# Optimization experiments

Hardware: AMD Instinct MI355X
Metric: run time of the kernel (lower is better)

Reference implementation:

```python
import jax, jax.numpy as jnp
import numpy as np

NUM_EXPERTS = 8
TOP_K = 2
LORA_ALPHA = 2.0
LORA_RANK = 16
D_MODEL = 2048
D_HIDDEN = 5632


def setup_inputs() -> dict:
    key = jax.random.key(0)
    ks = jax.random.split(key, 11)
    B, S, D, H, E, R = 2, 1024, D_MODEL, D_HIDDEN, NUM_EXPERTS, LORA_RANK
    sd = 1.0 / np.sqrt(D)
    sh = 1.0 / np.sqrt(H)
    x = jax.random.normal(ks[0], (B, S, D), jnp.float32)
    gate_w = jax.random.normal(ks[1], (E, D), jnp.float32) * sd   # router Linear(D->E), no bias
    w_up = jax.random.normal(ks[2], (H, D), jnp.float32) * sd     # up_proj.weight
    w_gate = jax.random.normal(ks[3], (H, D), jnp.float32) * sd   # gate_proj.weight
    w_down = jax.random.normal(ks[4], (D, H), jnp.float32) * sh   # down_proj.weight
    up_A = jax.random.normal(ks[5], (E, R, D), jnp.float32) * sd
    up_B = jax.random.normal(ks[6], (E, H, R), jnp.float32) * 0.02
    gate_A = jax.random.normal(ks[7], (E, R, D), jnp.float32) * sd
    gate_B = jax.random.normal(ks[8], (E, H, R), jnp.float32) * 0.02
    down_A = jax.random.normal(ks[9], (E, R, H), jnp.float32) * sh
    down_B = jax.random.normal(ks[10], (E, D, R), jnp.float32) * 0.02
    return {"x": x, "gate_w": gate_w, "w_up": w_up, "w_gate": w_gate,
            "w_down": w_down, "up_A": up_A, "up_B": up_B,
            "gate_A": gate_A, "gate_B": gate_B, "down_A": down_A, "down_B": down_B}


def reference(x, gate_w, w_up, w_gate, w_down, up_A, up_B, gate_A, gate_B, down_A, down_B):
    B, S, D = x.shape
    H = w_up.shape[0]
    # router: logits [B,S,E], top-k over experts (last dim)
    gate_logits = jnp.einsum('bsd,ed->bse', x, gate_w)
    topw, sel = jax.lax.top_k(gate_logits, TOP_K)            # [B,S,k]
    # NOTE: source applies softmax over dim=1 (the SEQUENCE axis) -- reproduced faithfully
    topw = jax.nn.softmax(topw.astype(jnp.float32), axis=1).astype(x.dtype)
    xt = x.reshape(-1, D)                                    # [T, D]
    wf = topw.reshape(-1, TOP_K)                             # [T, k]
    sf = sel.reshape(-1, TOP_K)                              # [T, k]
    # shared base projections computed once for all tokens
    base_up = xt @ w_up.T                                    # [T, H]
    base_gate = xt @ w_gate.T                                # [T, H]
    mixed_h = jnp.zeros((xt.shape[0], H), x.dtype)
    lora_down = jnp.zeros_like(xt)
    # loop over fixed small expert count; low-rank LoRA deltas applied without
    # materializing full merged weights (same math by linearity of matmul)
    for e in range(NUM_EXPERTS):
        c = jnp.sum(jnp.where(sf == e, wf, 0.0), axis=1)     # [T] routing weight (0 if not routed)
        lo_up = LORA_ALPHA * ((xt @ up_A[e].T) @ up_B[e].T)
        lo_gate = LORA_ALPHA * ((xt @ gate_A[e].T) @ gate_B[e].T)
        h_e = jax.nn.silu(base_up + lo_up) * (base_gate + lo_gate)  # [T, H]
        ch = c[:, None] * h_e
        mixed_h = mixed_h + ch
        lora_down = lora_down + LORA_ALPHA * ((ch @ down_A[e].T) @ down_B[e].T)
    out = mixed_h @ w_down.T + lora_down                     # base down GEMM done once on mixed hidden
    return out.reshape(B, S, D)
```

## Files before the change

### kernel.cpp

```cpp
#include <hip/hip_runtime.h>
#include <hip/hip_fp16.h>
#include <cmath>

#define TOKENS 2048
#define DMODEL 2048
#define DHID   5632
#define NEXP   8
#define RANK   16
#define LALPHA 2.0f

typedef __attribute__((ext_vector_type(4))) float f32x4;
typedef __attribute__((ext_vector_type(8))) short s16x8;
typedef __attribute__((ext_vector_type(4))) short s16x4;
typedef __attribute__((ext_vector_type(8))) _Float16 f16x8;

__device__ __forceinline__ short f2bf(float f){
  unsigned u = __float_as_uint(f);
  u += 0x7fffu + ((u >> 16) & 1u);
  return (short)(u >> 16);
}
__device__ __forceinline__ short f2h(float f){
  return (short)__half_as_ushort(__float2half(f));
}

struct Stage { const short* s0; const short* s1; short* d0; short* d1; };

__device__ __forceinline__ Stage mk_stage(const short* g, long ld, short* t, int tid){
  Stage st;
  const int L0 = tid,      r0 = L0>>2, c0 = ((L0&3) - (r0>>1)) & 3;
  const int L1 = 256+tid,  r1 = L1>>2, c1 = ((L1&3) - (r1>>1)) & 3;
  st.s0 = g + (long)r0*ld + c0*8;  st.d0 = t + L0*8;
  st.s1 = g + (long)r1*ld + c1*8;  st.d1 = t + L1*8;
  return st;
}
__device__ __forceinline__ void do_stage(const Stage& st, int k0){
  __builtin_amdgcn_global_load_lds((const __attribute__((address_space(1))) void*)(st.s0 + k0),
                                   (__attribute__((address_space(3))) void*)st.d0, 16, 0, 0);
  __builtin_amdgcn_global_load_lds((const __attribute__((address_space(1))) void*)(st.s1 + k0),
                                   (__attribute__((address_space(3))) void*)st.d1, 16, 0, 0);
}
__device__ __forceinline__ s16x8 fragb(const short* t, int row, int quad){
  const int p = (quad + (row>>1)) & 3;
  return *(const s16x8*)(t + (row*4 + p)*8);
}

struct Stage64 { const short* g; short* t; int off[4]; int dof; };

__device__ __forceinline__ Stage64 mk_stage64(const short* g, long ld, short* t, int tid){
  Stage64 st; st.g = g; st.t = t;
  #pragma unroll
  for(int p=0;p<4;p++){
    const int L = p*256 + tid;
    const int r = L>>3, cp = L&7;
    const int c = (cp - (r&7)) & 7;
    st.off[p] = r*(int)ld + c*8;
  }
  st.dof = tid*8;
  return st;
}
__device__ __forceinline__ void do_stage64(const Stage64& st, int k0){
  #pragma unroll
  for(int p=0;p<4;p++)
    __builtin_amdgcn_global_load_lds(
      (const __attribute__((address_space(1))) void*)(st.g + st.off[p] + k0),
      (__attribute__((address_space(3))) void*)(st.t + st.dof + p*2048), 16, 0, 0);
}
__device__ __forceinline__ s16x8 fragb64(const short* t, int row, int ksub, int quad){
  const int c = ksub*4 + quad;
  const int p = (c + (row&7)) & 7;
  return *(const s16x8*)(t + (row*8 + p)*8);
}
__device__ __forceinline__ f16x8 fragh64(const short* t, int row, int ksub, int quad){
  const int c = ksub*4 + quad;
  const int p = (c + (row&7)) & 7;
  return *(const f16x8*)(t + (row*8 + p)*8);
}

__global__ void k_cast(const float* __restrict__ x, const float* __restrict__ w_up,
                       const float* __restrict__ w_gate, const float* __restrict__ w_down,
                       const float* __restrict__ upA, const float* __restrict__ gateA,
                       const float* __restrict__ downA, const float* __restrict__ upB,
                       const float* __restrict__ gateB, const float* __restrict__ downB,
                       short* __restrict__ xb, short* __restrict__ wub, short* __restrict__ wgb,
                       short* __restrict__ wdb, short* __restrict__ daA, short* __restrict__ acat,
                       short* __restrict__ upBcat, short* __restrict__ gateBcat, short* __restrict__ wdbcat){
  const long e0 = 4194304, e1 = 15728640, e2 = 27262976, e3 = 38797312;
  const long e4 = 39518208, e5 = 40042496, e6 = 40763392, e7 = 41484288, e8 = 41746432;
  const long i = ((long)blockIdx.x*256 + threadIdx.x) * 4;
  if(i >= e8) return;
  const float* src; short* dst; long l; int fp16 = 0;
  if(i < e0){ src = x; dst = xb; l = i; }
  else if(i < e1){ src = w_up; dst = wub; l = i - e0; }
  else if(i < e2){ src = w_gate; dst = wgb; l = i - e1; }
  else if(i < e3){ src = w_down; dst = wdb; l = i - e2; }
  else if(i < e4){ src = downA; dst = daA; l = i - e3; }
  else if(i < e5){
    l = i - e4;
    const long c = l>>11;
    const long e = c>>5, pj = (c>>4)&1, r = c&15;
    src = (pj ? gateA : upA) + ((e*RANK + r)<<11) + (l&2047) - l;
    dst = acat;
  }
  else if(i < e6){
    l = i - e5;
    const long h = l>>7, c = l&127, e = c>>4, r = c&15;
    src = upB + ((e*DHID + h)*RANK + r) - l;
    dst = upBcat; fp16 = 1;
  }
  else if(i < e7){
    l = i - e6;
    const long h = l>>7, c = l&127, e = c>>4, r = c&15;
    src = gateB + ((e*DHID + h)*RANK + r) - l;
    dst = gateBcat; fp16 = 1;
  }
  else {
    l = i - e7;
    const long d = l>>7, c = l&127, e = c>>4, r = c&15;
    src = downB + ((e*DMODEL + d)*RANK + r) - l;
    dst = wdbcat; fp16 = 1;
  }
  const float4 v = *(const float4*)(src + l);
  s16x4 o;
  if(fp16){ o[0]=f2h(v.x); o[1]=f2h(v.y); o[2]=f2h(v.z); o[3]=f2h(v.w); }
  else    { o[0]=f2bf(v.x); o[1]=f2bf(v.y); o[2]=f2bf(v.z); o[3]=f2bf(v.w); }
  *(s16x4*)(dst + l) = o;
}

__global__ void k_router(const float* __restrict__ x, const float* __restrict__ gw,
                         int* __restrict__ sel, float* __restrict__ topv){
  const int t = blockIdx.x*4 + (threadIdx.x>>6);
  const int lane = threadIdx.x & 63;
  const float* xr = x + (long)t * DMODEL;
  float acc[NEXP];
  #pragma unroll
  for(int e=0;e<NEXP;e++) acc[e]=0.f;
  #pragma unroll
  for(int it=0; it<8; it++){
    const int d = it*256 + lane*4;
    const float4 xv = *(const float4*)(xr + d);
    #pragma unroll
    for(int e=0;e<NEXP;e++){
      const float4 wv = *(const float4*)(gw + e*DMODEL + d);
      acc[e] += xv.x*wv.x + xv.y*wv.y + xv.z*wv.z + xv.w*wv.w;
    }
  }
  #pragma unroll
  for(int e=0;e<NEXP;e++){
    #pragma unroll
    for(int off=32; off; off>>=1) acc[e] += __shfl_down(acc[e], off, 64);
  }
  if(lane==0){
    int i0=0;
    #pragma unroll
    for(int e=1;e<NEXP;e++) if(acc[e]>acc[i0]) i0=e;
    int i1=-1;
    #pragma unroll
    for(int e=0;e<NEXP;e++){ if(e==i0) continue; if(i1<0 || acc[e]>acc[i1]) i1=e; }
    sel[t*2+0]=i0; sel[t*2+1]=i1;
    topv[t*2+0]=acc[i0]; topv[t*2+1]=acc[i1];
  }
}

__global__ void k_softmax(const float* __restrict__ topv, float* __restrict__ cw){
  const int b = blockIdx.x >> 1, k = blockIdx.x & 1;
  const int base = b*1024;
  __shared__ float red[256];
  float v[4];
  float mx = -1e30f;
  #pragma unroll
  for(int i=0;i<4;i++){
    int s = threadIdx.x + i*256;
    v[i] = topv[(base+s)*2 + k];
    mx = fmaxf(mx, v[i]);
  }
  red[threadIdx.x]=mx; __syncthreads();
  for(int o=128;o;o>>=1){ if(threadIdx.x<o) red[threadIdx.x]=fmaxf(red[threadIdx.x],red[threadIdx.x+o]); __syncthreads(); }
  mx = red[0]; __syncthreads();
  float sum=0.f;
  #pragma unroll
  for(int i=0;i<4;i++){ v[i]=__expf(v[i]-mx); sum+=v[i]; }
  red[threadIdx.x]=sum; __syncthreads();
  for(int o=128;o;o>>=1){ if(threadIdx.x<o) red[threadIdx.x]+=red[threadIdx.x+o]; __syncthreads(); }
  const float inv = 1.f/red[0];
  #pragma unroll
  for(int i=0;i<4;i++){
    int s = threadIdx.x + i*256;
    cw[(base+s)*2+k] = v[i]*inv;
  }
}

__global__ __launch_bounds__(256,2) void k_rank(
    const short* __restrict__ xb, const short* __restrict__ acat, float* __restrict__ Rall){
  __shared__ __align__(16) short At[8192];
  __shared__ __align__(16) short Bt[8192];
  const int c0 = blockIdx.x*128, t0 = blockIdx.y*128;
  const int kbeg = blockIdx.z*256;
  const int tid = threadIdx.x, lane = tid&63, wave = tid>>6;
  const int wm=(wave>>1)*64, wn=(wave&1)*64, fr=lane&15, quad=lane>>4;
  f32x4 acc[4][4];
  #pragma unroll
  for(int i=0;i<4;i++)
    #pragma unroll
    for(int j=0;j<4;j++) acc[i][j]=(f32x4){0.f,0.f,0.f,0.f};
  const Stage64 sA = mk_stage64(xb + (long)t0*DMODEL, DMODEL, At, tid);
  const Stage64 sB = mk_stage64(acat + (long)c0*DMODEL, DMODEL, Bt, tid);
  for(int k0=kbeg; k0<kbeg+256; k0+=64){
    do_stage64(sA, k0); do_stage64(sB, k0);
    __syncthreads();
    #pragma unroll
    for(int s=0;s<2;s++){
      s16x8 af[4];
      #pragma unroll
      for(int i=0;i<4;i++) af[i] = fragb64(At, wm + i*16 + fr, s, quad);
      #pragma unroll
      for(int j=0;j<4;j++){
        const s16x8 bf = fragb64(Bt, wn + j*16 + fr, s, quad);
        #pragma unroll
        for(int i=0;i<4;i++)
          acc[i][j] = __builtin_amdgcn_mfma_f32_16x16x32_bf16(af[i], bf, acc[i][j], 0,0,0);
      }
    }
    __syncthreads();
  }
  #pragma unroll
  for(int i=0;i<4;i++)
    #pragma unroll
    for(int j=0;j<4;j++){
      const int rbase = wm + i*16 + quad*4, col = wn + j*16 + fr;
      #pragma unroll
      for(int reg=0;reg<4;reg++)
        atomicAdd(&Rall[(long)(t0+rbase+reg)*256 + c0 + col], acc[i][j][reg]);
    }
}

__global__ void k_rsel(const float* __restrict__ Rall, const int* __restrict__ sel,
                       short* __restrict__ RselU, short* __restrict__ RselG){
  const int idx = blockIdx.x*256 + threadIdx.x;
  const int c = idx & 127, t = (idx>>7) & (TOKENS-1), k = idx>>18;
  const int e = c>>4, r = c&15;
  const int s = sel[t*2+k];
  const int m = (e==s);
  RselU[idx] = f2h(m ? LALPHA*Rall[(long)t*256 + e*32 + r]      : 0.f);
  RselG[idx] = f2h(m ? LALPHA*Rall[(long)t*256 + e*32 + 16 + r] : 0.f);
}

__global__ __launch_bounds__(256,2) void k_lora(
    const short* __restrict__ RselU, const short* __restrict__ RselG,
    const short* __restrict__ upBcat, const short* __restrict__ gateBcat,
    short* __restrict__ LF){
  __shared__ __align__(16) short At[8192];
  __shared__ __align__(16) short Gt[8192];
  __shared__ __align__(16) short Bt[8192];
  const int h0 = blockIdx.x*128, t0 = blockIdx.y*128;
  const short* Rsel = blockIdx.z ? RselG : RselU;
  const short* Bcat = blockIdx.z ? gateBcat : upBcat;
  const int tid = threadIdx.x, lane = tid&63, wave = tid>>6;
  const int wm=(wave>>1)*64, wn=(wave&1)*64, fr=lane&15, quad=lane>>4;
  f32x4 l0[4][4], l1[4][4];
  #pragma unroll
  for(int i=0;i<4;i++)
    #pragma unroll
    for(int j=0;j<4;j++){ l0[i][j]=(f32x4){0.f,0.f,0.f,0.f}; l1[i][j]=l0[i][j]; }
  const Stage64 sB  = mk_stage64(Bcat + (long)h0*128, 128, Bt, tid);
  const Stage64 sR0 = mk_stage64(Rsel + (long)t0*128, 128, At, tid);
  const Stage64 sR1 = mk_stage64(Rsel + ((long)TOKENS + t0)*128, 128, Gt, tid);
  for(int k0=0; k0<128; k0+=64){
    do_stage64(sB, k0); do_stage64(sR0, k0); do_stage64(sR1, k0);
    __syncthreads();
    #pragma unroll
    for(int s=0;s<2;s++){
      f16x8 a0[4], a1[4];
      #pragma unroll
      for(int i=0;i<4;i++){ a0[i] = fragh64(At, wm + i*16 + fr, s, quad);
                            a1[i] = fragh64(Gt, wm + i*16 + fr, s, quad); }
      #pragma unroll
      for(int j=0;j<4;j++){
        const f16x8 bf = fragh64(Bt, wn + j*16 + fr, s, quad);
        #pragma unroll
        for(int i=0;i<4;i++){
          l0[i][j] = __builtin_amdgcn_mfma_f32_16x16x32_f16(a0[i], bf, l0[i][j], 0,0,0);
          l1[i][j] = __builtin_amdgcn_mfma_f32_16x16x32_f16(a1[i], bf, l1[i][j], 0,0,0);
        }
      }
    }
    __syncthreads();
  }
  short* o = LF + (((long)(blockIdx.y*44 + blockIdx.x)*256 + tid)*256) + blockIdx.z*128;
  #pragma unroll
  for(int i=0;i<4;i++){
    s16x8 p0a, p0b, p1a, p1b;
    #pragma unroll
    for(int r=0;r<4;r++){
      p0a[r]   = f2h(l0[i][0][r]); p0a[4+r] = f2h(l0[i][1][r]);
      p0b[r]   = f2h(l0[i][2][r]); p0b[4+r] = f2h(l0[i][3][r]);
      p1a[r]   = f2h(l1[i][0][r]); p1a[4+r] = f2h(l1[i][1][r]);
      p1b[r]   = f2h(l1[i][2][r]); p1b[4+r] = f2h(l1[i][3][r]);
    }
    *(s16x8*)(o + i*16)          = p0a;
    *(s16x8*)(o + i*16 + 8)      = p0b;
    *(s16x8*)(o + 64 + i*16)     = p1a;
    *(s16x8*)(o + 64 + i*16 + 8) = p1b;
  }
}

__global__ __launch_bounds__(256,2) void k_main(
    const short* __restrict__ xb, const short* __restrict__ wub, const short* __restrict__ wgb,
    const short* __restrict__ LF,
    const float* __restrict__ cw, unsigned short* __restrict__ ch, unsigned short* __restrict__ chsum){
  __shared__ __align__(16) short At[8192];
  __shared__ __align__(16) short Ut[8192];
  __shared__ __align__(16) short Gt[8192];
  __shared__ float cwv[128][2];
  const int h0 = blockIdx.x*128, t0 = blockIdx.y*128;
  const int tid = threadIdx.x, lane = tid&63, wave = tid>>6;
  const int wm=(wave>>1)*64, wn=(wave&1)*64, fr=lane&15, quad=lane>>4;
  { const int tl = tid>>1, k = tid&1; cwv[tl][k] = cw[(t0+tl)*2 + k]; }
  f32x4 au[4][4], ag[4][4];
  #pragma unroll
  for(int i=0;i<4;i++)
    #pragma unroll
    for(int j=0;j<4;j++){ au[i][j]=(f32x4){0.f,0.f,0.f,0.f}; ag[i][j]=au[i][j]; }
  const Stage64 sA = mk_stage64(xb + (long)t0*DMODEL, DMODEL, At, tid);
  const Stage64 sU = mk_stage64(wub + (long)h0*DMODEL, DMODEL, Ut, tid);
  const Stage64 sG = mk_stage64(wgb + (long)h0*DMODEL, DMODEL, Gt, tid);
  for(int k0=0; k0<DMODEL; k0+=64){
    do_stage64(sA, k0); do_stage64(sU, k0); do_stage64(sG, k0);
    __syncthreads();
    #pragma unroll
    for(int s=0;s<2;s++){
      s16x8 af[4];
      #pragma unroll
      for(int i=0;i<4;i++) af[i] = fragb64(At, wm + i*16 + fr, s, quad);
      #pragma unroll
      for(int j=0;j<4;j++){
        const s16x8 bu = fragb64(Ut, wn + j*16 + fr, s, quad);
        const s16x8 bg = fragb64(Gt, wn + j*16 + fr, s, quad);
        #pragma unroll
        for(int i=0;i<4;i++){
          au[i][j] = __builtin_amdgcn_mfma_f32_16x16x32_bf16(af[i], bu, au[i][j], 0,0,0);
          ag[i][j] = __builtin_amdgcn_mfma_f32_16x16x32_bf16(af[i], bg, ag[i][j], 0,0,0);
        }
      }
    }
    __syncthreads();
  }
  const short* Lf = LF + (((long)(blockIdx.y*44 + blockIdx.x)*256 + tid)*256);
  #pragma unroll
  for(int i=0;i<4;i++){
    f16x8 Uv0[2], Uv1[2], Gv0[2], Gv1[2];
    Uv0[0] = *(const f16x8*)(Lf + i*16);        Uv0[1] = *(const f16x8*)(Lf + i*16 + 8);
    Uv1[0] = *(const f16x8*)(Lf + 64 + i*16);   Uv1[1] = *(const f16x8*)(Lf + 64 + i*16 + 8);
    Gv0[0] = *(const f16x8*)(Lf + 128 + i*16);  Gv0[1] = *(const f16x8*)(Lf + 128 + i*16 + 8);
    Gv1[0] = *(const f16x8*)(Lf + 192 + i*16);  Gv1[1] = *(const f16x8*)(Lf + 192 + i*16 + 8);
    #pragma unroll
    for(int reg=0;reg<4;reg++){
      const int tl = wm + i*16 + quad*4 + reg;
      const float c0 = cwv[tl][0], c1 = cwv[tl][1];
      const long row0 = (long)(t0+tl)*DHID + h0;
      const long row1 = ((long)TOKENS + t0+tl)*DHID + h0;
      unsigned short* r0 = ch + row0;
      unsigned short* r1 = ch + row1;
      unsigned short* rs = chsum + row0;
      #pragma unroll
      for(int j=0;j<4;j++){
        const int hl = wn + j*16 + fr;
        const int q = (j&1)*4 + reg, hv = j>>1;
        const float u0 = au[i][j][reg] + (float)Uv0[hv][q];
        const float g0 = ag[i][j][reg] + (float)Gv0[hv][q];
        const float h0v = (u0 / (1.f + __expf(-u0))) * g0;
        const float u1 = au[i][j][reg] + (float)Uv1[hv][q];
        const float g1 = ag[i][j][reg] + (float)Gv1[hv][q];
        const float h1v = (u1 / (1.f + __expf(-u1))) * g1;
        const float v0 = c0*h0v, v1 = c1*h1v;
        r0[hl] = (unsigned short)f2bf(v0);
        r1[hl] = (unsigned short)f2bf(v1);
        rs[hl] = (unsigned short)f2bf(v0+v1);
      }
    }
  }
}

__global__ __launch_bounds__(256,4) void k_rd(
    const unsigned short* __restrict__ ch, const short* __restrict__ daA,
    float* __restrict__ RD){
  __shared__ __align__(16) short At[4096];
  __shared__ __align__(16) short Bt[4096];
  const int slot = blockIdx.x>>4, ks = blockIdx.x&15;
  const int t0 = blockIdx.y*128;
  const int tid = threadIdx.x, lane = tid&63, wave = tid>>6;
  const int wm=(wave>>1)*64, wn=(wave&1)*64, fr=lane&15, quad=lane>>4;
  f32x4 acc[4][4];
  #pragma unroll
  for(int i=0;i<4;i++)
    #pragma unroll
    for(int j=0;j<4;j++) acc[i][j]=(f32x4){0.f,0.f,0.f,0.f};
  const Stage sA = mk_stage((const short*)ch + ((long)slot*TOKENS + t0)*DHID, DHID, At, tid);
  const Stage sB = mk_stage(daA, DHID, Bt, tid);
  const int kbeg = ks*352;
  for(int kk=0; kk<352; kk+=32){
    do_stage(sA, kbeg+kk); do_stage(sB, kbeg+kk);
    __syncthreads();
    s16x8 af[4];
    #pragma unroll
    for(int i=0;i<4;i++) af[i] = fragb(At, wm + i*16 + fr, quad);
    #pragma unroll
    for(int j=0;j<4;j++){
      const s16x8 bf = fragb(Bt, wn + j*16 + fr, quad);
      #pragma unroll
      for(int i=0;i<4;i++)
        acc[i][j] = __builtin_amdgcn_mfma_f32_16x16x32_bf16(af[i], bf, acc[i][j], 0,0,0);
    }
    __syncthreads();
  }
  #pragma unroll
  for(int i=0;i<4;i++)
    #pragma unroll
    for(int j=0;j<4;j++){
      const int rbase = wm + i*16 + quad*4, col = wn + j*16 + fr;
      #pragma unroll
      for(int reg=0;reg<4;reg++)
        atomicAdd(&RD[((long)(t0+rbase+reg)*2 + slot)*128 + col], acc[i][j][reg]);
    }
}

__global__ void k_scatter(const float* __restrict__ RD, const int* __restrict__ sel,
                          __half* __restrict__ RDhat){
  const int idx = blockIdx.x*256 + threadIdx.x;
  const int t = idx>>7, c = idx&127, e = c>>4;
  const int s0 = sel[t*2], s1 = sel[t*2+1];
  float v = 0.f;
  if(e == s0) v = LALPHA * RD[((long)t*2+0)*128 + c];
  else if(e == s1) v = LALPHA * RD[((long)t*2+1)*128 + c];
  RDhat[idx] = __float2half(v);
}

__global__ __launch_bounds__(256,2) void k_down(
    const unsigned short* __restrict__ chsum, const short* __restrict__ wdb,
    const short* __restrict__ RDhat, const short* __restrict__ wdbcat,
    float* __restrict__ out){
  __shared__ __align__(16) short At[8192];
  __shared__ __align__(16) short Bt[8192];
  const int d0 = blockIdx.x*128, t0 = blockIdx.y*128, ks = blockIdx.z;
  const int tid = threadIdx.x, lane = tid&63, wave = tid>>6;
  const int wm=(wave>>1)*64, wn=(wave&1)*64, fr=lane&15, quad=lane>>4;
  f32x4 acc[4][4];
  #pragma unroll
  for(int i=0;i<4;i++)
    #pragma unroll
    for(int j=0;j<4;j++) acc[i][j]=(f32x4){0.f,0.f,0.f,0.f};
  const Stage64 sA = mk_stage64((const short*)chsum + (long)t0*DHID, DHID, At, tid);
  const Stage64 sB = mk_stage64(wdb + (long)d0*DHID, DHID, Bt, tid);
  const int kbeg = ks*2816;
  for(int kk=0; kk<2816; kk+=64){
    do_stage64(sA, kbeg+kk); do_stage64(sB, kbeg+kk);
    __syncthreads();
    #pragma unroll
    for(int s=0;s<2;s++){
      s16x8 af[4];
      #pragma unroll
      for(int i=0;i<4;i++) af[i] = fragb64(At, wm + i*16 + fr, s, quad);
      #pragma unroll
      for(int j=0;j<4;j++){
        const s16x8 bf = fragb64(Bt, wn + j*16 + fr, s, quad);
        #pragma unroll
        for(int i=0;i<4;i++)
          acc[i][j] = __builtin_amdgcn_mfma_f32_16x16x32_bf16(af[i], bf, acc[i][j], 0,0,0);
      }
    }
    __syncthreads();
  }
  if(ks == 0){
    const Stage64 sAh = mk_stage64(RDhat + (long)t0*128, 128, At, tid);
    const Stage64 sBh = mk_stage64(wdbcat + (long)d0*128, 128, Bt, tid);
    for(int k0=0; k0<128; k0+=64){
      do_stage64(sAh, k0); do_stage64(sBh, k0);
      __syncthreads();
      #pragma unroll
      for(int s=0;s<2;s++){
        f16x8 af[4];
        #pragma unroll
        for(int i=0;i<4;i++) af[i] = fragh64(At, wm + i*16 + fr, s, quad);
        #pragma unroll
        for(int j=0;j<4;j++){
          const f16x8 bf = fragh64(Bt, wn + j*16 + fr, s, quad);
          #pragma unroll
          for(int i=0;i<4;i++)
            acc[i][j] = __builtin_amdgcn_mfma_f32_16x16x32_f16(af[i], bf, acc[i][j], 0,0,0);
        }
      }
      __syncthreads();
    }
  }
  #pragma unroll
  for(int i=0;i<4;i++)
    #pragma unroll
    for(int j=0;j<4;j++){
      const int rbase = wm + i*16 + quad*4, col = wn + j*16 + fr;
      #pragma unroll
      for(int reg=0;reg<4;reg++)
        atomicAdd(&out[(long)(t0+rbase+reg)*DMODEL + d0 + col], acc[i][j][reg]);
    }
}

extern "C" void kernel_launch(void* const* d_in, const int* in_sizes, int n_in,
                              void* d_out, int out_size, void* d_ws, size_t ws_size,
                              hipStream_t stream){
  (void)in_sizes; (void)n_in; (void)out_size; (void)ws_size;
  const float* x      = (const float*)d_in[0];
  const float* gate_w = (const float*)d_in[1];
  const float* w_up   = (const float*)d_in[2];
  const float* w_gate = (const float*)d_in[3];
  const float* w_down = (const float*)d_in[4];
  const float* up_A   = (const float*)d_in[5];
  const float* up_B   = (const float*)d_in[6];
  const float* gate_A = (const float*)d_in[7];
  const float* gate_B = (const float*)d_in[8];
  const float* down_A = (const float*)d_in[9];
  const float* down_B = (const float*)d_in[10];
  float* out = (float*)d_out;

  char* ws = (char*)d_ws;
  size_t off = 0;
  auto alloc = [&](size_t bytes){ void* p = ws + off; off += (bytes + 255) & ~(size_t)255; return p; };
  short* xb       = (short*)alloc((size_t)TOKENS*DMODEL*2);
  short* wub      = (short*)alloc((size_t)DHID*DMODEL*2);
  short* wgb      = (short*)alloc((size_t)DHID*DMODEL*2);
  short* wdb      = (short*)alloc((size_t)DMODEL*DHID*2);
  short* daA      = (short*)alloc((size_t)128*DHID*2);
  short* acat     = (short*)alloc((size_t)256*DMODEL*2);
  short* upBcat   = (short*)alloc((size_t)DHID*128*2);
  short* gateBcat = (short*)alloc((size_t)DHID*128*2);
  short* wdbcat   = (short*)alloc((size_t)DMODEL*128*2);
  unsigned short* ch    = (unsigned short*)alloc((size_t)2*TOKENS*DHID*2);
  unsigned short* chsum = (unsigned short*)alloc((size_t)TOKENS*DHID*2);
  short* LF     = (short*)alloc((size_t)704*256*256*2);
  float* Rall   = (float*)alloc((size_t)TOKENS*256*4);
  short* RselU  = (short*)alloc((size_t)2*TOKENS*128*2);
  short* RselG  = (short*)alloc((size_t)2*TOKENS*128*2);
  float* RD     = (float*)alloc((size_t)TOKENS*2*128*4);
  __half* RDhat = (__half*)alloc((size_t)TOKENS*128*2);
  int*   sel    = (int*)alloc((size_t)TOKENS*2*4);
  float* topv   = (float*)alloc((size_t)TOKENS*2*4);
  float* cw     = (float*)alloc((size_t)TOKENS*2*4);

  (void)hipMemsetAsync(RD, 0, (size_t)TOKENS*2*128*4, stream);
  (void)hipMemsetAsync(Rall, 0, (size_t)TOKENS*256*4, stream);
  (void)hipMemsetAsync(out, 0, (size_t)TOKENS*DMODEL*4, stream);
  k_cast<<<40768, 256, 0, stream>>>(x, w_up, w_gate, w_down, up_A, gate_A, down_A,
                                    up_B, gate_B, down_B,
                                    xb, wub, wgb, wdb, daA, acat, upBcat, gateBcat, wdbcat);
  k_router<<<512, 256, 0, stream>>>(x, gate_w, sel, topv);
  k_softmax<<<4, 256, 0, stream>>>(topv, cw);
  k_rank<<<dim3(2,16,8), 256, 0, stream>>>(xb, acat, Rall);
  k_rsel<<<2048, 256, 0, stream>>>(Rall, sel, RselU, RselG);
  k_lora<<<dim3(44,16,2), 256, 0, stream>>>(RselU, RselG, upBcat, gateBcat, LF);
  k_main<<<dim3(44,16), 256, 0, stream>>>(xb, wub, wgb, LF, cw, ch, chsum);
  k_rd<<<dim3(32,16), 256, 0, stream>>>(ch, daA, RD);
  k_scatter<<<1024, 256, 0, stream>>>(RD, sel, RDhat);
  k_down<<<dim3(16,16,2), 256, 0, stream>>>(chsum, wdb, (const short*)RDhat, wdbcat, out);
}
```

Before: 581.9 us.

## Double-buffer LDS tiles in main and down GEMMs with K=32 steps

Converts the fused up/gate GEMM and the down-projection GEMM from single-buffered 64-wide K tiles to double-buffered 32-wide K tiles. The next tile's global-to-LDS load is issued before the MFMAs on the current tile, so each iteration needs only one barrier. The per-block LoRA fragment buffer is also re-laid out so each thread's 16-byte stores and loads are coalesced across threads rather than strided by 512 bytes. The cost is twice as many loop iterations and barriers per K length, with a smaller tile per step.

```diff
diff --git a/kernel.cpp b/kernel.cpp
--- a/kernel.cpp
+++ b/kernel.cpp
@@ -23,25 +23,29 @@
   return (short)__half_as_ushort(__float2half(f));
 }
 
-struct Stage { const short* s0; const short* s1; short* d0; short* d1; };
-
-__device__ __forceinline__ Stage mk_stage(const short* g, long ld, short* t, int tid){
-  Stage st;
+struct Src2 { const short* s0; const short* s1; };
+
+__device__ __forceinline__ Src2 mk_src(const short* g, long ld, int tid){
+  Src2 st;
   const int L0 = tid,      r0 = L0>>2, c0 = ((L0&3) - (r0>>1)) & 3;
   const int L1 = 256+tid,  r1 = L1>>2, c1 = ((L1&3) - (r1>>1)) & 3;
-  st.s0 = g + (long)r0*ld + c0*8;  st.d0 = t + L0*8;
-  st.s1 = g + (long)r1*ld + c1*8;  st.d1 = t + L1*8;
+  st.s0 = g + (long)r0*ld + c0*8;
+  st.s1 = g + (long)r1*ld + c1*8;
   return st;
 }
-__device__ __forceinline__ void do_stage(const Stage& st, int k0){
+__device__ __forceinline__ void stage2(const Src2& st, int k0, short* t, int tid){
   __builtin_amdgcn_global_load_lds((const __attribute__((address_space(1))) void*)(st.s0 + k0),
-                                   (__attribute__((address_space(3))) void*)st.d0, 16, 0, 0);
+                                   (__attribute__((address_space(3))) void*)(t + tid*8), 16, 0, 0);
   __builtin_amdgcn_global_load_lds((const __attribute__((address_space(1))) void*)(st.s1 + k0),
-                                   (__attribute__((address_space(3))) void*)st.d1, 16, 0, 0);
+                                   (__attribute__((address_space(3))) void*)(t + (256+tid)*8), 16, 0, 0);
 }
 __device__ __forceinline__ s16x8 fragb(const short* t, int row, int quad){
   const int p = (quad + (row>>1)) & 3;
   return *(const s16x8*)(t + (row*4 + p)*8);
+}
+__device__ __forceinline__ f16x8 fragh(const short* t, int row, int quad){
+  const int p = (quad + (row>>1)) & 3;
+  return *(const f16x8*)(t + (row*4 + p)*8);
 }
 
 struct Stage64 { const short* g; short* t; int off[4]; int dof; };
@@ -285,7 +289,7 @@
     }
     __syncthreads();
   }
-  short* o = LF + (((long)(blockIdx.y*44 + blockIdx.x)*256 + tid)*256) + blockIdx.z*128;
+  short* o = LF + (long)(blockIdx.y*44 + blockIdx.x)*65536 + ((long)blockIdx.z*16*256 + tid)*8;
   #pragma unroll
   for(int i=0;i<4;i++){
     s16x8 p0a, p0b, p1a, p1b;
@@ -296,10 +300,10 @@
       p1a[r]   = f2h(l1[i][0][r]); p1a[4+r] = f2h(l1[i][1][r]);
       p1b[r]   = f2h(l1[i][2][r]); p1b[4+r] = f2h(l1[i][3][r]);
     }
-    *(s16x8*)(o + i*16)          = p0a;
-    *(s16x8*)(o + i*16 + 8)      = p0b;
-    *(s16x8*)(o + 64 + i*16)     = p1a;
-    *(s16x8*)(o + 64 + i*16 + 8) = p1b;
+    *(s16x8*)(o + (i*2+0)*2048)     = p0a;
+    *(s16x8*)(o + (i*2+1)*2048)     = p0b;
+    *(s16x8*)(o + (8 + i*2+0)*2048) = p1a;
+    *(s16x8*)(o + (8 + i*2+1)*2048) = p1b;
   }
 }
 
@@ -307,9 +311,9 @@
     const short* __restrict__ xb, const short* __restrict__ wub, const short* __restrict__ wgb,
     const short* __restrict__ LF,
     const float* __restrict__ cw, unsigned short* __restrict__ ch, unsigned short* __restrict__ chsum){
-  __shared__ __align__(16) short At[8192];
-  __shared__ __align__(16) short Ut[8192];
-  __shared__ __align__(16) short Gt[8192];
+  __shared__ __align__(16) short At[2][4096];
+  __shared__ __align__(16) short Ut[2][4096];
+  __shared__ __align__(16) short Gt[2][4096];
   __shared__ float cwv[128][2];
   const int h0 = blockIdx.x*128, t0 = blockIdx.y*128;
   const int tid = threadIdx.x, lane = tid&63, wave = tid>>6;
@@ -320,38 +324,44 @@
   for(int i=0;i<4;i++)
     #pragma unroll
     for(int j=0;j<4;j++){ au[i][j]=(f32x4){0.f,0.f,0.f,0.f}; ag[i][j]=au[i][j]; }
-  const Stage64 sA = mk_stage64(xb + (long)t0*DMODEL, DMODEL, At, tid);
-  const Stage64 sU = mk_stage64(wub + (long)h0*DMODEL, DMODEL, Ut, tid);
-  const Stage64 sG = mk_stage64(wgb + (long)h0*DMODEL, DMODEL, Gt, tid);
-  for(int k0=0; k0<DMODEL; k0+=64){
-    do_stage64(sA, k0); do_stage64(sU, k0); do_stage64(sG, k0);
-    __syncthreads();
-    #pragma unroll
-    for(int s=0;s<2;s++){
-      s16x8 af[4];
-      #pragma unroll
-      for(int i=0;i<4;i++) af[i] = fragb64(At, wm + i*16 + fr, s, quad);
-      #pragma unroll
-      for(int j=0;j<4;j++){
-        const s16x8 bu = fragb64(Ut, wn + j*16 + fr, s, quad);
-        const s16x8 bg = fragb64(Gt, wn + j*16 + fr, s, quad);
-        #pragma unroll
-        for(int i=0;i<4;i++){
-          au[i][j] = __builtin_amdgcn_mfma_f32_16x16x32_bf16(af[i], bu, au[i][j], 0,0,0);
-          ag[i][j] = __builtin_amdgcn_mfma_f32_16x16x32_bf16(af[i], bg, ag[i][j], 0,0,0);
-        }
+  const Src2 sA = mk_src(xb + (long)t0*DMODEL, DMODEL, tid);
+  const Src2 sU = mk_src(wub + (long)h0*DMODEL, DMODEL, tid);
+  const Src2 sG = mk_src(wgb + (long)h0*DMODEL, DMODEL, tid);
+  stage2(sA, 0, At[0], tid); stage2(sU, 0, Ut[0], tid); stage2(sG, 0, Gt[0], tid);
+  __syncthreads();
+  int cur = 0;
+  for(int k0=0; k0<DMODEL; k0+=32){
+    const int nxt = cur^1;
+    if(k0+32 < DMODEL){
+      stage2(sA, k0+32, At[nxt], tid);
+      stage2(sU, k0+32, Ut[nxt], tid);
+      stage2(sG, k0+32, Gt[nxt], tid);
+    }
+    __builtin_amdgcn_sched_barrier(0);
+    s16x8 af[4];
+    #pragma unroll
+    for(int i=0;i<4;i++) af[i] = fragb(At[cur], wm + i*16 + fr, quad);
+    #pragma unroll
+    for(int j=0;j<4;j++){
+      const s16x8 bu = fragb(Ut[cur], wn + j*16 + fr, quad);
+      const s16x8 bg = fragb(Gt[cur], wn + j*16 + fr, quad);
+      #pragma unroll
+      for(int i=0;i<4;i++){
+        au[i][j] = __builtin_amdgcn_mfma_f32_16x16x32_bf16(af[i], bu, au[i][j], 0,0,0);
+        ag[i][j] = __builtin_amdgcn_mfma_f32_16x16x32_bf16(af[i], bg, ag[i][j], 0,0,0);
       }
     }
     __syncthreads();
-  }
-  const short* Lf = LF + (((long)(blockIdx.y*44 + blockIdx.x)*256 + tid)*256);
+    cur = nxt;
+  }
+  const short* Lf = LF + (long)(blockIdx.y*44 + blockIdx.x)*65536 + (long)tid*8;
   #pragma unroll
   for(int i=0;i<4;i++){
     f16x8 Uv0[2], Uv1[2], Gv0[2], Gv1[2];
-    Uv0[0] = *(const f16x8*)(Lf + i*16);        Uv0[1] = *(const f16x8*)(Lf + i*16 + 8);
-    Uv1[0] = *(const f16x8*)(Lf + 64 + i*16);   Uv1[1] = *(const f16x8*)(Lf + 64 + i*16 + 8);
-    Gv0[0] = *(const f16x8*)(Lf + 128 + i*16);  Gv0[1] = *(const f16x8*)(Lf + 128 + i*16 + 8);
-    Gv1[0] = *(const f16x8*)(Lf + 192 + i*16);  Gv1[1] = *(const f16x8*)(Lf + 192 + i*16 + 8);
+    Uv0[0] = *(const f16x8*)(Lf + (i*2+0)*2048);       Uv0[1] = *(const f16x8*)(Lf + (i*2+1)*2048);
+    Uv1[0] = *(const f16x8*)(Lf + (8+i*2+0)*2048);     Uv1[1] = *(const f16x8*)(Lf + (8+i*2+1)*2048);
+    Gv0[0] = *(const f16x8*)(Lf + (16+i*2+0)*2048);    Gv0[1] = *(const f16x8*)(Lf + (16+i*2+1)*2048);
+    Gv1[0] = *(const f16x8*)(Lf + (24+i*2+0)*2048);    Gv1[1] = *(const f16x8*)(Lf + (24+i*2+1)*2048);
     #pragma unroll
     for(int reg=0;reg<4;reg++){
       const int tl = wm + i*16 + quad*4 + reg;
@@ -394,11 +404,11 @@
   for(int i=0;i<4;i++)
     #pragma unroll
     for(int j=0;j<4;j++) acc[i][j]=(f32x4){0.f,0.f,0.f,0.f};
-  const Stage sA = mk_stage((const short*)ch + ((long)slot*TOKENS + t0)*DHID, DHID, At, tid);
-  const Stage sB = mk_stage(daA, DHID, Bt, tid);
+  const Src2 sA = mk_src((const short*)ch + ((long)slot*TOKENS + t0)*DHID, DHID, tid);
+  const Src2 sB = mk_src(daA, DHID, tid);
   const int kbeg = ks*352;
   for(int kk=0; kk<352; kk+=32){
-    do_stage(sA, kbeg+kk); do_stage(sB, kbeg+kk);
+    stage2(sA, kbeg+kk, At, tid); stage2(sB, kbeg+kk, Bt, tid);
     __syncthreads();
     s16x8 af[4];
     #pragma unroll
@@ -438,8 +448,8 @@
     const unsigned short* __restrict__ chsum, const short* __restrict__ wdb,
     const short* __restrict__ RDhat, const short* __restrict__ wdbcat,
     float* __restrict__ out){
-  __shared__ __align__(16) short At[8192];
-  __shared__ __align__(16) short Bt[8192];
+  __shared__ __align__(16) short At[2][4096];
+  __shared__ __align__(16) short Bt[2][4096];
   const int d0 = blockIdx.x*128, t0 = blockIdx.y*128, ks = blockIdx.z;
   const int tid = threadIdx.x, lane = tid&63, wave = tid>>6;
   const int wm=(wave>>1)*64, wn=(wave&1)*64, fr=lane&15, quad=lane>>4;
@@ -448,47 +458,56 @@
   for(int i=0;i<4;i++)
     #pragma unroll
     for(int j=0;j<4;j++) acc[i][j]=(f32x4){0.f,0.f,0.f,0.f};
-  const Stage64 sA = mk_stage64((const short*)chsum + (long)t0*DHID, DHID, At, tid);
-  const Stage64 sB = mk_stage64(wdb + (long)d0*DHID, DHID, Bt, tid);
+  const Src2 sA = mk_src((const short*)chsum + (long)t0*DHID, DHID, tid);
+  const Src2 sB = mk_src(wdb + (long)d0*DHID, DHID, tid);
   const int kbeg = ks*2816;
-  for(int kk=0; kk<2816; kk+=64){
-    do_stage64(sA, kbeg+kk); do_stage64(sB, kbeg+kk);
-    __syncthreads();
-    #pragma unroll
-    for(int s=0;s<2;s++){
-      s16x8 af[4];
-      #pragma unroll
-      for(int i=0;i<4;i++) af[i] = fragb64(At, wm + i*16 + fr, s, quad);
+  stage2(sA, kbeg, At[0], tid); stage2(sB, kbeg, Bt[0], tid);
+  __syncthreads();
+  int cur = 0;
+  for(int kk=0; kk<2816; kk+=32){
+    const int nxt = cur^1;
+    if(kk+32 < 2816){
+      stage2(sA, kbeg+kk+32, At[nxt], tid);
+      stage2(sB, kbeg+kk+32, Bt[nxt], tid);
+    }
+    __builtin_amdgcn_sched_barrier(0);
+    s16x8 af[4];
+    #pragma unroll
+    for(int i=0;i<4;i++) af[i] = fragb(At[cur], wm + i*16 + fr, quad);
+    #pragma unroll
+    for(int j=0;j<4;j++){
+      const s16x8 bf = fragb(Bt[cur], wn + j*16 + fr, quad);
+      #pragma unroll
+      for(int i=0;i<4;i++)
+        acc[i][j] = __builtin_amdgcn_mfma_f32_16x16x32_bf16(af[i], bf, acc[i][j], 0,0,0);
+    }
+    __syncthreads();
+    cur = nxt;
+  }
+  if(ks == 0){
+    const Src2 sAh = mk_src(RDhat + (long)t0*128, 128, tid);
+    const Src2 sBh = mk_src(wdbcat + (long)d0*128, 128, tid);
+    stage2(sAh, 0, At[cur], tid); stage2(sBh, 0, Bt[cur], tid);
+    __syncthreads();
+    for(int k0=0; k0<128; k0+=32){
+      const int nxt = cur^1;
+      if(k0+32 < 128){
+        stage2(sAh, k0+32, At[nxt], tid);
+        stage2(sBh, k0+32, Bt[nxt], tid);
+      }
+      __builtin_amdgcn_sched_barrier(0);
+      f16x8 af[4];
+      #pragma unroll
+      for(int i=0;i<4;i++) af[i] = fragh(At[cur], wm + i*16 + fr, quad);
       #pragma unroll
       for(int j=0;j<4;j++){
-        const s16x8 bf = fragb64(Bt, wn + j*16 + fr, s, quad);
+        const f16x8 bf = fragh(Bt[cur], wn + j*16 + fr, quad);
         #pragma unroll
         for(int i=0;i<4;i++)
-          acc[i][j] = __builtin_amdgcn_mfma_f32_16x16x32_bf16(af[i], bf, acc[i][j], 0,0,0);
-      }
-    }
-    __syncthreads();
-  }
-  if(ks == 0){
-    const Stage64 sAh = mk_stage64(RDhat + (long)t0*128, 128, At, tid);
-    const Stage64 sBh = mk_stage64(wdbcat + (long)d0*128, 128, Bt, tid);
-    for(int k0=0; k0<128; k0+=64){
-      do_stage64(sAh, k0); do_stage64(sBh, k0);
-      __syncthreads();
-      #pragma unroll
-      for(int s=0;s<2;s++){
-        f16x8 af[4];
-        #pragma unroll
-        for(int i=0;i<4;i++) af[i] = fragh64(At, wm + i*16 + fr, s, quad);
-        #pragma unroll
-        for(int j=0;j<4;j++){
-          const f16x8 bf = fragh64(Bt, wn + j*16 + fr, s, quad);
-          #pragma unroll
-          for(int i=0;i<4;i++)
-            acc[i][j] = __builtin_amdgcn_mfma_f32_16x16x32_f16(af[i], bf, acc[i][j], 0,0,0);
-        }
+          acc[i][j] = __builtin_amdgcn_mfma_f32_16x16x32_f16(af[i], bf, acc[i][j], 0,0,0);
       }
       __syncthreads();
+      cur = nxt;
     }
   }
   #pragma unroll
@@ -533,7 +552,7 @@
   short* wdbcat   = (short*)alloc((size_t)DMODEL*128*2);
   unsigned short* ch    = (unsigned short*)alloc((size_t)2*TOKENS*DHID*2);
   unsigned short* chsum = (unsigned short*)alloc((size_t)TOKENS*DHID*2);
-  short* LF     = (short*)alloc((size_t)704*256*256*2);
+  short* LF     = (short*)alloc((size_t)704*65536*2);
   float* Rall   = (float*)alloc((size_t)TOKENS*256*4);
   short* RselU  = (short*)alloc((size_t)2*TOKENS*128*2);
   short* RselG  = (short*)alloc((size_t)2*TOKENS*128*2);
```

Result: faster. 538.9 us (-7.4%).
